# Performance work log

Hardware: AMD Instinct MI355X
Metric: run time of the kernel (lower is better)

## Reference

```python
import jax, jax.numpy as jnp
import numpy as np

N = 20000      # nodes
E = 320000     # edges (before self loops)
F_IN = 256     # num_node_features
H = 8          # heads
C = 64         # dim_h per head
B = 64         # graphs in batch
NC = 10        # num_classes
HID = H * C    # 512


def setup_inputs() -> dict:
    key = jax.random.key(0)
    ks = jax.random.split(key, 20)
    def glorot(k, shape, fan):
        return jax.random.normal(k, shape, jnp.float32) / np.sqrt(fan)
    inp = {
        'x': jax.random.normal(ks[0], (N, F_IN), jnp.float32),
        'edge_index': jax.random.randint(ks[1], (2, E), 0, N),
        'batch': jnp.sort(jax.random.randint(ks[2], (N,), 0, B)),
        # conv1: F_IN -> H*C
        'W1': glorot(ks[3], (F_IN, HID), F_IN),
        'a_src1': glorot(ks[4], (H, C), C),
        'a_dst1': glorot(ks[5], (H, C), C),
        'b1': jnp.zeros((HID,), jnp.float32),
        # conv2: HID -> H*C
        'W2': glorot(ks[6], (HID, HID), HID),
        'a_src2': glorot(ks[7], (H, C), C),
        'a_dst2': glorot(ks[8], (H, C), C),
        'b2': jnp.zeros((HID,), jnp.float32),
        # conv3: HID -> H*C
        'W3': glorot(ks[9], (HID, HID), HID),
        'a_src3': glorot(ks[10], (H, C), C),
        'a_dst3': glorot(ks[11], (H, C), C),
        'b3': jnp.zeros((HID,), jnp.float32),
        # final classifier
        'Wl': glorot(ks[12], (HID, NC), HID),
        'bl': jnp.zeros((NC,), jnp.float32),
    }
    return inp


def _gat_conv(x, src, dst, W, a_src, a_dst, b):
    """PyG GATConv (concat=True, negative_slope=0.2). src/dst include self loops."""
    xt = (x @ W).reshape(-1, H, C)                      # [N, H, C]
    al_s = jnp.einsum('nhc,hc->nh', xt, a_src)          # [N, H]
    al_d = jnp.einsum('nhc,hc->nh', xt, a_dst)
    e = jax.nn.leaky_relu(al_s[src] + al_d[dst], 0.2)   # [E', H]
    m = jax.ops.segment_max(e, dst, num_segments=N)     # segment softmax (stable)
    m = jax.lax.stop_gradient(jnp.where(jnp.isfinite(m), m, 0.0))
    p = jnp.exp(e - m[dst])
    s = jax.ops.segment_sum(p, dst, num_segments=N)
    alpha = p / (s[dst] + 1e-16)                        # [E', H]
    msg = xt[src] * alpha[..., None]                    # [E', H, C]
    out = jax.ops.segment_sum(msg, dst, num_segments=N) # [N, H, C]
    return out.reshape(-1, HID) + b


def reference(x, edge_index, batch, W1, a_src1, a_dst1, b1,
              W2, a_src2, a_dst2, b2, W3, a_src3, a_dst3, b3, Wl, bl):
    loop = jnp.arange(N, dtype=edge_index.dtype)
    src = jnp.concatenate([edge_index[0], loop])        # add_self_loops=True
    dst = jnp.concatenate([edge_index[1], loop])

    h = jax.nn.elu(_gat_conv(x, src, dst, W1, a_src1, a_dst1, b1))
    h = jax.nn.elu(_gat_conv(h, src, dst, W2, a_src2, a_dst2, b2))
    h = jax.nn.elu(_gat_conv(h, src, dst, W3, a_src3, a_dst3, b3))

    # global mean pool over graphs
    cnt = jax.ops.segment_sum(jnp.ones((N,), h.dtype), batch, num_segments=B)
    hG = jax.ops.segment_sum(h, batch, num_segments=B) / jnp.clip(cnt, 1.0)[:, None]

    # dropout p=0.5 is identity in eval mode
    logits = hG @ Wl + bl
    return hG, jax.nn.softmax(logits, axis=1)
```

## Files before the change

### kernel.cpp

```cpp
#include <hip/hip_runtime.h>
#include <hip/hip_bf16.h>
#include <math.h>

#define N_NODES  20000
#define E_EDGES  320000
#define E_TOT    (E_EDGES + N_NODES)
#define F_INF    256
#define HEADS    8
#define CDIM     64
#define HID      512
#define B_GRAPHS 64
#define NCLS     10
#define M_PAD    20096
#define NSCAN    20

typedef __attribute__((ext_vector_type(8))) short short8;
typedef __attribute__((ext_vector_type(4))) float f32x4;

__device__ inline unsigned short f2bf(float x) {
    unsigned u = __builtin_bit_cast(unsigned, x);
    u += 0x7fff + ((u >> 16) & 1);
    return (unsigned short)(u >> 16);
}
__device__ inline float bf2f(unsigned short h) {
    unsigned u = ((unsigned)h) << 16;
    return __builtin_bit_cast(float, u);
}

#define GLOAD_LDS16(g, l) __builtin_amdgcn_global_load_lds(                     \
        (const __attribute__((address_space(1))) void*)(g),                     \
        (__attribute__((address_space(3))) void*)(l), 16, 0, 0)

__global__ __launch_bounds__(256) void zero_ints(int* p, int n) {
    int i = blockIdx.x * 256 + threadIdx.x;
    if (i < n) p[i] = 0;
}

__global__ __launch_bounds__(256) void zero_pad_rows(unsigned short* hi, unsigned short* lo) {
    int i = blockIdx.x * 256 + threadIdx.x;
    const int tot = (M_PAD - N_NODES) * HID;
    if (i < tot) {
        hi[(size_t)N_NODES * HID + i] = 0;
        lo[(size_t)N_NODES * HID + i] = 0;
    }
}

__global__ __launch_bounds__(256) void split_pad(const float* __restrict__ src,
                                                 unsigned short* __restrict__ hi,
                                                 unsigned short* __restrict__ lo,
                                                 int M, int K, long total) {
    long i = ((long)blockIdx.x * 256 + threadIdx.x) * 4;
    if (i >= total) return;
    int row = (int)(i / K);
    float4 v = make_float4(0.f, 0.f, 0.f, 0.f);
    if (row < M) v = *(const float4*)(src + i);
    ushort4 h, l;
    h.x = f2bf(v.x); l.x = f2bf(v.x - bf2f(h.x));
    h.y = f2bf(v.y); l.y = f2bf(v.y - bf2f(h.y));
    h.z = f2bf(v.z); l.z = f2bf(v.z - bf2f(h.z));
    h.w = f2bf(v.w); l.w = f2bf(v.w - bf2f(h.w));
    *(ushort4*)(hi + i) = h;
    *(ushort4*)(lo + i) = l;
}

__global__ __launch_bounds__(256) void transpose_split_B(const float* __restrict__ B,
                                                         unsigned short* __restrict__ Bthi,
                                                         unsigned short* __restrict__ Btlo,
                                                         int K) {
    __shared__ float t[32][33];
    int n0 = blockIdx.x * 32, k0 = blockIdx.y * 32;
    int tx = threadIdx.x & 31, ty = threadIdx.x >> 5;
    for (int i = ty; i < 32; i += 8) t[i][tx] = B[(size_t)(k0 + i) * HID + n0 + tx];
    __syncthreads();
    for (int i = ty; i < 32; i += 8) {
        float v = t[tx][i];
        unsigned short h = f2bf(v);
        unsigned short l = f2bf(v - bf2f(h));
        Bthi[(size_t)(n0 + i) * K + k0 + tx] = h;
        Btlo[(size_t)(n0 + i) * K + k0 + tx] = l;
    }
}

__global__ __launch_bounds__(256) void gemm_mfma(const unsigned short* __restrict__ Ahi,
                                                 const unsigned short* __restrict__ Alo,
                                                 const unsigned short* __restrict__ Bhi,
                                                 const unsigned short* __restrict__ Blo,
                                                 const float* __restrict__ a_src,
                                                 const float* __restrict__ a_dst,
                                                 unsigned short* __restrict__ xtb,
                                                 float* __restrict__ al_s,
                                                 float* __restrict__ al_d,
                                                 int M, int K) {
    __shared__ short AsHi[4096], AsLo[4096], BsHi[4096], BsLo[4096];
    const int tid = threadIdx.x;
    const int w = tid >> 6, lane = tid & 63;
    const int wr = w >> 1, wc = w & 1;
    const int row0 = blockIdx.x * 128, col0 = blockIdx.y * 128;

    long offA[2], offB[2];
    int ldsU[2];
#pragma unroll
    for (int i = 0; i < 2; ++i) {
        int u = w * 128 + i * 64 + lane;
        int row = u >> 2;
        int kg = (u & 3) ^ (row & 3);
        offA[i] = ((long)(row0 + row) * K + kg * 8) * 2;
        offB[i] = ((long)(col0 + row) * K + kg * 8) * 2;
        ldsU[i] = (w * 128 + i * 64) * 8;
    }

    const int r16 = lane & 15, kg = lane >> 4;
    int aOff[4], bOff[4];
#pragma unroll
    for (int i = 0; i < 4; ++i) {
        int row = wr * 64 + i * 16 + r16;
        aOff[i] = (row * 4 + (kg ^ (row & 3))) * 16;
        int col = wc * 64 + i * 16 + r16;
        bOff[i] = (col * 4 + (kg ^ (col & 3))) * 16;
    }

    const char* pAhi = (const char*)Ahi;
    const char* pAlo = (const char*)Alo;
    const char* pBhi = (const char*)Bhi;
    const char* pBlo = (const char*)Blo;

    f32x4 acc[4][4] = {};

    for (int kk = 0; kk < K; kk += 32) {
        long kb = (long)kk * 2;
        __syncthreads();
#pragma unroll
        for (int i = 0; i < 2; ++i) {
            GLOAD_LDS16(pAhi + offA[i] + kb, AsHi + ldsU[i]);
            GLOAD_LDS16(pAlo + offA[i] + kb, AsLo + ldsU[i]);
            GLOAD_LDS16(pBhi + offB[i] + kb, BsHi + ldsU[i]);
            GLOAD_LDS16(pBlo + offB[i] + kb, BsLo + ldsU[i]);
        }
        __syncthreads();

        short8 ah[4], al[4], bh[4], bl[4];
#pragma unroll
        for (int i = 0; i < 4; ++i) {
            ah[i] = *(const short8*)((const char*)AsHi + aOff[i]);
            al[i] = *(const short8*)((const char*)AsLo + aOff[i]);
            bh[i] = *(const short8*)((const char*)BsHi + bOff[i]);
            bl[i] = *(const short8*)((const char*)BsLo + bOff[i]);
        }
#pragma unroll
        for (int i = 0; i < 4; ++i)
#pragma unroll
            for (int j = 0; j < 4; ++j) {
                acc[i][j] = __builtin_amdgcn_mfma_f32_16x16x32_bf16(ah[i], bh[j], acc[i][j], 0, 0, 0);
                acc[i][j] = __builtin_amdgcn_mfma_f32_16x16x32_bf16(ah[i], bl[j], acc[i][j], 0, 0, 0);
                acc[i][j] = __builtin_amdgcn_mfma_f32_16x16x32_bf16(al[i], bh[j], acc[i][j], 0, 0, 0);
            }
    }

    const int h = (col0 >> 6) + wc;
    float asv[4], adv[4];
#pragma unroll
    for (int j = 0; j < 4; ++j) {
        asv[j] = a_src[h * CDIM + j * 16 + r16];
        adv[j] = a_dst[h * CDIM + j * 16 + r16];
    }
#pragma unroll
    for (int i = 0; i < 4; ++i) {
        int rbase = row0 + wr * 64 + i * 16 + (lane >> 4) * 4;
#pragma unroll
        for (int r = 0; r < 4; ++r) {
            float ss = acc[i][0][r] * asv[0] + acc[i][1][r] * asv[1]
                     + acc[i][2][r] * asv[2] + acc[i][3][r] * asv[3];
            float dd = acc[i][0][r] * adv[0] + acc[i][1][r] * adv[1]
                     + acc[i][2][r] * adv[2] + acc[i][3][r] * adv[3];
#pragma unroll
            for (int off = 1; off < 16; off <<= 1) {
                ss += __shfl_xor(ss, off);
                dd += __shfl_xor(dd, off);
            }
            int row = rbase + r;
            if ((lane & 15) == 0 && row < M) {
                al_s[row * HEADS + h] = ss;
                al_d[row * HEADS + h] = dd;
            }
        }
#pragma unroll
        for (int j = 0; j < 4; ++j) {
            int col = col0 + wc * 64 + j * 16 + r16;
#pragma unroll
            for (int r = 0; r < 4; ++r)
                if (rbase + r < M) xtb[(size_t)(rbase + r) * HID + col] = f2bf(acc[i][j][r]);
        }
    }
}

__global__ __launch_bounds__(256) void count_edges(const int* __restrict__ ei,
                                                   int* __restrict__ counts) {
    int e = blockIdx.x * 256 + threadIdx.x;
    if (e < E_TOT) {
        int dst = (e < E_EDGES) ? ei[E_EDGES + e] : (e - E_EDGES);
        atomicAdd(&counts[dst], 1);
    }
}

__global__ __launch_bounds__(1024) void scan_local(const int* __restrict__ counts,
                                                   int* __restrict__ incl,
                                                   int* __restrict__ bsum) {
    __shared__ int s[1024];
    int tid = threadIdx.x;
    int i = blockIdx.x * 1024 + tid;
    int v = (i < N_NODES) ? counts[i] : 0;
    s[tid] = v;
    __syncthreads();
    for (int off = 1; off < 1024; off <<= 1) {
        int t = (tid >= off) ? s[tid - off] : 0;
        __syncthreads();
        s[tid] += t;
        __syncthreads();
    }
    if (i < N_NODES) incl[i] = s[tid];
    if (tid == 1023) bsum[blockIdx.x] = s[1023];
}

__global__ __launch_bounds__(64) void scan_bsums(const int* __restrict__ bsum,
                                                 int* __restrict__ bpre) {
    int lane = threadIdx.x;
    int v = (lane < NSCAN) ? bsum[lane] : 0;
    int incl = v;
#pragma unroll
    for (int off = 1; off < 32; off <<= 1) {
        int t = __shfl_up(incl, off);
        if (lane >= off) incl += t;
    }
    if (lane < NSCAN) bpre[lane] = incl - v;
}

__global__ __launch_bounds__(1024) void scan_finalize(const int* __restrict__ counts,
                                                      const int* __restrict__ incl,
                                                      const int* __restrict__ bpre,
                                                      int* __restrict__ offsets,
                                                      int* __restrict__ cursor) {
    int i = blockIdx.x * 1024 + threadIdx.x;
    if (i < N_NODES) {
        int inc = incl[i] + bpre[blockIdx.x];
        offsets[i + 1] = inc;
        cursor[i] = inc - counts[i];
    }
    if (i == 0) offsets[0] = 0;
}

__global__ __launch_bounds__(256) void scatter_edges(const int* __restrict__ ei,
                                                     int* __restrict__ cursor,
                                                     int* __restrict__ csr) {
    int e = blockIdx.x * 256 + threadIdx.x;
    if (e < E_TOT) {
        int dst = (e < E_EDGES) ? ei[E_EDGES + e] : (e - E_EDGES);
        int pos = atomicAdd(&cursor[dst], 1);
        csr[pos] = e;
    }
}

__global__ __launch_bounds__(256) void gat_aggregate4(const unsigned short* __restrict__ xtb,
                                                      const float* __restrict__ al_s,
                                                      const float* __restrict__ al_d,
                                                      const int* __restrict__ offsets,
                                                      const int* __restrict__ csr,
                                                      const int* __restrict__ ei,
                                                      const float* __restrict__ bias,
                                                      unsigned short* __restrict__ outHi,
                                                      unsigned short* __restrict__ outLo) {
    const int lane = threadIdx.x & 63;
    const int n = blockIdx.x * 4 + (threadIdx.x >> 6);
    const int h = lane >> 3;
    const int c0 = lane * 8;
    const int beg = offsets[n];
    const int deg = offsets[n + 1] - beg;
    const float aldv = al_d[n * HEADS + h];

    float acc[8] = {};
    float psum = 0.f;

#pragma unroll 4
    for (int i = 0; i < deg; ++i) {
        int e = csr[beg + i];
        int srcn = (e < E_EDGES) ? ei[e] : (e - E_EDGES);
        float ev = al_s[srcn * HEADS + h] + aldv;
        ev = (ev >= 0.f) ? ev : 0.2f * ev;
        float p = expf(ev);
        psum += p;
        short8 row = *(const short8*)(xtb + (size_t)srcn * HID + c0);
#pragma unroll
        for (int j = 0; j < 8; ++j)
            acc[j] = fmaf(p, bf2f((unsigned short)row[j]), acc[j]);
    }

    const float inv = 1.f / (psum + 1e-16f);
    float4 b0 = *(const float4*)(bias + c0);
    float4 b1 = *(const float4*)(bias + c0 + 4);
    float bv[8] = { b0.x, b0.y, b0.z, b0.w, b1.x, b1.y, b1.z, b1.w };
    short8 h8, l8;
#pragma unroll
    for (int j = 0; j < 8; ++j) {
        float v = acc[j] * inv + bv[j];
        v = (v > 0.f) ? v : expm1f(v);
        unsigned short hi = f2bf(v);
        h8[j] = (short)hi;
        l8[j] = (short)f2bf(v - bf2f(hi));
    }
    size_t o = (size_t)n * HID + c0;
    *(short8*)(outHi + o) = h8;
    *(short8*)(outLo + o) = l8;
}

__global__ __launch_bounds__(128) void find_bounds(const int* __restrict__ batch,
                                                   int* __restrict__ bounds) {
    int b = threadIdx.x;
    if (b <= B_GRAPHS) {
        int lo = 0, hi = N_NODES;
        while (lo < hi) {
            int mid = (lo + hi) >> 1;
            if (batch[mid] < b) lo = mid + 1; else hi = mid;
        }
        bounds[b] = lo;
    }
}

__global__ __launch_bounds__(256) void pool_partial(const unsigned short* __restrict__ hHi,
                                                    const unsigned short* __restrict__ hLo,
                                                    const int* __restrict__ bounds,
                                                    float* __restrict__ partial) {
    const int b = blockIdx.x, y = blockIdx.y, k = blockIdx.z;
    const int s = bounds[b], cnt = bounds[b + 1] - s;
    const int ns = s + (cnt * k) / 4;
    const int ne = s + (cnt * (k + 1)) / 4;
    const int t = threadIdx.x;
    const int chp = t & 31;
    const int nl = t >> 5;

    float a0 = 0.f, a1 = 0.f;
    for (int n = ns + nl; n < ne; n += 8) {
        size_t off = (size_t)n * HID + y * 64 + chp * 2;
        unsigned vh = *(const unsigned*)(hHi + off);
        unsigned vl = *(const unsigned*)(hLo + off);
        a0 += bf2f((unsigned short)(vh & 0xffff)) + bf2f((unsigned short)(vl & 0xffff));
        a1 += bf2f((unsigned short)(vh >> 16)) + bf2f((unsigned short)(vl >> 16));
    }
    __shared__ float red[4][32][2];
    a0 += __shfl_xor(a0, 32);
    a1 += __shfl_xor(a1, 32);
    if ((t & 63) < 32) { red[t >> 6][chp][0] = a0; red[t >> 6][chp][1] = a1; }
    __syncthreads();
    if (t < 64) {
        int cp = t >> 1, c = t & 1;
        float v = red[0][cp][c] + red[1][cp][c] + red[2][cp][c] + red[3][cp][c];
        partial[(((size_t)k * B_GRAPHS + b) * 8 + y) * 64 + cp * 2 + c] = v;
    }
}

__global__ __launch_bounds__(512) void pool_final(const float* __restrict__ partial,
                                                  const int* __restrict__ bounds,
                                                  float* __restrict__ hG) {
    const int b = blockIdx.x, t = threadIdx.x;
    float v = 0.f;
#pragma unroll
    for (int k = 0; k < 4; ++k)
        v += partial[((size_t)k * B_GRAPHS + b) * HID + t];
    float cnt = fmaxf((float)(bounds[b + 1] - bounds[b]), 1.0f);
    hG[b * HID + t] = v / cnt;
}

__global__ __launch_bounds__(64) void classifier_kernel(const float* __restrict__ hG,
                                                        const float* __restrict__ Wl,
                                                        const float* __restrict__ bl,
                                                        float* __restrict__ outP) {
    int b = blockIdx.x;
    int tid = threadIdx.x;
    __shared__ float row[HID];
    __shared__ float logit[NCLS];
    for (int j = tid; j < HID; j += 64) row[j] = hG[b * HID + j];
    __syncthreads();
    if (tid < NCLS) {
        float acc = bl[tid];
        for (int j = 0; j < HID; ++j) acc += row[j] * Wl[j * NCLS + tid];
        logit[tid] = acc;
    }
    __syncthreads();
    if (tid == 0) {
        float mx = logit[0];
        for (int k = 1; k < NCLS; ++k) mx = fmaxf(mx, logit[k]);
        float ssum = 0.f, ex[NCLS];
        for (int k = 0; k < NCLS; ++k) { ex[k] = expf(logit[k] - mx); ssum += ex[k]; }
        for (int k = 0; k < NCLS; ++k) outP[b * NCLS + k] = ex[k] / ssum;
    }
}

extern "C" void kernel_launch(void* const* d_in, const int* in_sizes, int n_in,
                              void* d_out, int out_size, void* d_ws, size_t ws_size,
                              hipStream_t stream) {
    const float* x     = (const float*)d_in[0];
    const int*   ei    = (const int*)d_in[1];
    const int*   batch = (const int*)d_in[2];
    const float* W[3]  = { (const float*)d_in[3], (const float*)d_in[7],  (const float*)d_in[11] };
    const float* as_[3] = { (const float*)d_in[4], (const float*)d_in[8],  (const float*)d_in[12] };
    const float* ad_[3] = { (const float*)d_in[5], (const float*)d_in[9],  (const float*)d_in[13] };
    const float* bb[3] = { (const float*)d_in[6], (const float*)d_in[10], (const float*)d_in[14] };
    const float* Wl    = (const float*)d_in[15];
    const float* bl    = (const float*)d_in[16];

    char* ws = (char*)d_ws;
    unsigned short* A1hi = (unsigned short*)ws;      ws += (size_t)M_PAD * F_INF * 2;
    unsigned short* A1lo = (unsigned short*)ws;      ws += (size_t)M_PAD * F_INF * 2;
    unsigned short* A2hi = (unsigned short*)ws;      ws += (size_t)M_PAD * HID * 2;
    unsigned short* A2lo = (unsigned short*)ws;      ws += (size_t)M_PAD * HID * 2;
    unsigned short* Bthi = (unsigned short*)ws;      ws += (size_t)HID * HID * 2;
    unsigned short* Btlo = (unsigned short*)ws;      ws += (size_t)HID * HID * 2;
    unsigned short* xtb  = (unsigned short*)ws;      ws += (size_t)N_NODES * HID * 2;
    float* als  = (float*)ws;                        ws += (size_t)N_NODES * HEADS * 4;
    float* ald  = (float*)ws;                        ws += (size_t)N_NODES * HEADS * 4;
    float* partial = (float*)ws;                     ws += (size_t)4 * B_GRAPHS * HID * 4;
    int* counts  = (int*)ws;                         ws += (size_t)N_NODES * 4;
    int* incl    = (int*)ws;                         ws += (size_t)N_NODES * 4;
    int* bsum    = (int*)ws;                         ws += 32 * 4;
    int* bpre    = (int*)ws;                         ws += 32 * 4;
    int* offsets = (int*)ws;                         ws += (size_t)(N_NODES + 1) * 4;
    int* cursor  = (int*)ws;                         ws += (size_t)N_NODES * 4;
    int* csr     = (int*)ws;                         ws += (size_t)E_TOT * 4;
    int* bounds  = (int*)ws;                         ws += (size_t)(B_GRAPHS + 1) * 4;

    float* hG = (float*)d_out;
    float* probs = (float*)d_out + (size_t)B_GRAPHS * HID;

    zero_ints<<<(N_NODES + 255) / 256, 256, 0, stream>>>(counts, N_NODES);
    count_edges<<<(E_TOT + 255) / 256, 256, 0, stream>>>(ei, counts);
    scan_local<<<NSCAN, 1024, 0, stream>>>(counts, incl, bsum);
    scan_bsums<<<1, 64, 0, stream>>>(bsum, bpre);
    scan_finalize<<<NSCAN, 1024, 0, stream>>>(counts, incl, bpre, offsets, cursor);
    scatter_edges<<<(E_TOT + 255) / 256, 256, 0, stream>>>(ei, cursor, csr);
    find_bounds<<<1, 128, 0, stream>>>(batch, bounds);
    zero_pad_rows<<<((M_PAD - N_NODES) * HID + 255) / 256, 256, 0, stream>>>(A2hi, A2lo);

    dim3 ggrid(M_PAD / 128, HID / 128);

    {
        long totA = (long)M_PAD * F_INF;
        split_pad<<<(int)(totA / 4 / 256), 256, 0, stream>>>(x, A1hi, A1lo, N_NODES, F_INF, totA);
        transpose_split_B<<<dim3(HID / 32, F_INF / 32), 256, 0, stream>>>(W[0], Bthi, Btlo, F_INF);
        gemm_mfma<<<ggrid, 256, 0, stream>>>(A1hi, A1lo, Bthi, Btlo, as_[0], ad_[0],
                                             xtb, als, ald, N_NODES, F_INF);
        gat_aggregate4<<<N_NODES / 4, 256, 0, stream>>>(xtb, als, ald, offsets, csr, ei, bb[0], A2hi, A2lo);
    }

    for (int L = 1; L < 3; ++L) {
        transpose_split_B<<<dim3(HID / 32, HID / 32), 256, 0, stream>>>(W[L], Bthi, Btlo, HID);
        gemm_mfma<<<ggrid, 256, 0, stream>>>(A2hi, A2lo, Bthi, Btlo, as_[L], ad_[L],
                                             xtb, als, ald, N_NODES, HID);
        gat_aggregate4<<<N_NODES / 4, 256, 0, stream>>>(xtb, als, ald, offsets, csr, ei, bb[L], A2hi, A2lo);
    }

    {
        dim3 pgrid(B_GRAPHS, 8, 4);
        pool_partial<<<pgrid, 256, 0, stream>>>(A2hi, A2lo, bounds, partial);
        pool_final<<<B_GRAPHS, 512, 0, stream>>>(partial, bounds, hG);
    }
    classifier_kernel<<<B_GRAPHS, 64, 0, stream>>>(hG, Wl, bl, probs);
}
```

Measured before the change: 454.9 us.

## Double-buffer GEMM LDS tiles and store source ids directly in CSR

```diff
diff --git a/kernel.cpp b/kernel.cpp
--- a/kernel.cpp
+++ b/kernel.cpp
@@ -91,7 +91,7 @@
                                                  float* __restrict__ al_s,
                                                  float* __restrict__ al_d,
                                                  int M, int K) {
-    __shared__ short AsHi[4096], AsLo[4096], BsHi[4096], BsLo[4096];
+    __shared__ short AsHi[2][4096], AsLo[2][4096], BsHi[2][4096], BsLo[2][4096];
     const int tid = threadIdx.x;
     const int w = tid >> 6, lane = tid & 63;
     const int wr = w >> 1, wc = w & 1;
@@ -126,35 +126,52 @@
 
     f32x4 acc[4][4] = {};
 
-    for (int kk = 0; kk < K; kk += 32) {
-        long kb = (long)kk * 2;
-        __syncthreads();
-#pragma unroll
-        for (int i = 0; i < 2; ++i) {
-            GLOAD_LDS16(pAhi + offA[i] + kb, AsHi + ldsU[i]);
-            GLOAD_LDS16(pAlo + offA[i] + kb, AsLo + ldsU[i]);
-            GLOAD_LDS16(pBhi + offB[i] + kb, BsHi + ldsU[i]);
-            GLOAD_LDS16(pBlo + offB[i] + kb, BsLo + ldsU[i]);
-        }
-        __syncthreads();
-
-        short8 ah[4], al[4], bh[4], bl[4];
-#pragma unroll
-        for (int i = 0; i < 4; ++i) {
-            ah[i] = *(const short8*)((const char*)AsHi + aOff[i]);
-            al[i] = *(const short8*)((const char*)AsLo + aOff[i]);
-            bh[i] = *(const short8*)((const char*)BsHi + bOff[i]);
-            bl[i] = *(const short8*)((const char*)BsLo + bOff[i]);
-        }
-#pragma unroll
-        for (int i = 0; i < 4; ++i)
-#pragma unroll
-            for (int j = 0; j < 4; ++j) {
-                acc[i][j] = __builtin_amdgcn_mfma_f32_16x16x32_bf16(ah[i], bh[j], acc[i][j], 0, 0, 0);
-                acc[i][j] = __builtin_amdgcn_mfma_f32_16x16x32_bf16(ah[i], bl[j], acc[i][j], 0, 0, 0);
-                acc[i][j] = __builtin_amdgcn_mfma_f32_16x16x32_bf16(al[i], bh[j], acc[i][j], 0, 0, 0);
-            }
-    }
+#define STAGE(buf, kk) do {                                                      \
+        long kb = (long)(kk) * 64;                                               \
+        _Pragma("unroll")                                                        \
+        for (int i_ = 0; i_ < 2; ++i_) {                                         \
+            GLOAD_LDS16(pAhi + offA[i_] + kb, &AsHi[buf][ldsU[i_]]);             \
+            GLOAD_LDS16(pAlo + offA[i_] + kb, &AsLo[buf][ldsU[i_]]);             \
+            GLOAD_LDS16(pBhi + offB[i_] + kb, &BsHi[buf][ldsU[i_]]);             \
+            GLOAD_LDS16(pBlo + offB[i_] + kb, &BsLo[buf][ldsU[i_]]);             \
+        }                                                                        \
+    } while (0)
+
+#define COMPUTE(buf) do {                                                        \
+        short8 fah[4], fal[4], fbh[4], fbl[4];                                   \
+        _Pragma("unroll")                                                        \
+        for (int i_ = 0; i_ < 4; ++i_) {                                         \
+            fah[i_] = *(const short8*)((const char*)AsHi[buf] + aOff[i_]);       \
+            fal[i_] = *(const short8*)((const char*)AsLo[buf] + aOff[i_]);       \
+            fbh[i_] = *(const short8*)((const char*)BsHi[buf] + bOff[i_]);       \
+            fbl[i_] = *(const short8*)((const char*)BsLo[buf] + bOff[i_]);       \
+        }                                                                        \
+        _Pragma("unroll")                                                        \
+        for (int i_ = 0; i_ < 4; ++i_)                                           \
+            _Pragma("unroll")                                                    \
+            for (int j_ = 0; j_ < 4; ++j_) {                                     \
+                acc[i_][j_] = __builtin_amdgcn_mfma_f32_16x16x32_bf16(fah[i_], fbh[j_], acc[i_][j_], 0, 0, 0); \
+                acc[i_][j_] = __builtin_amdgcn_mfma_f32_16x16x32_bf16(fah[i_], fbl[j_], acc[i_][j_], 0, 0, 0); \
+                acc[i_][j_] = __builtin_amdgcn_mfma_f32_16x16x32_bf16(fal[i_], fbh[j_], acc[i_][j_], 0, 0, 0); \
+            }                                                                    \
+    } while (0)
+
+    const int NS = K >> 5;
+    STAGE(0, 0);
+    asm volatile("s_waitcnt vmcnt(0)" ::: "memory");
+    __builtin_amdgcn_s_barrier();
+    int cur = 0;
+    for (int t = 0; t < NS - 1; ++t) {
+        STAGE(cur ^ 1, t + 1);
+        COMPUTE(cur);
+        asm volatile("s_waitcnt vmcnt(0)" ::: "memory");
+        __builtin_amdgcn_s_barrier();
+        cur ^= 1;
+    }
+    COMPUTE(cur);
+
+#undef STAGE
+#undef COMPUTE
 
     const int h = (col0 >> 6) + wc;
     float asv[4], adv[4];
@@ -253,9 +270,11 @@
                                                      int* __restrict__ csr) {
     int e = blockIdx.x * 256 + threadIdx.x;
     if (e < E_TOT) {
-        int dst = (e < E_EDGES) ? ei[E_EDGES + e] : (e - E_EDGES);
+        int srcn, dst;
+        if (e < E_EDGES) { srcn = ei[e]; dst = ei[E_EDGES + e]; }
+        else             { srcn = dst = e - E_EDGES; }
         int pos = atomicAdd(&cursor[dst], 1);
-        csr[pos] = e;
+        csr[pos] = srcn;
     }
 }
 
@@ -264,7 +283,6 @@
                                                       const float* __restrict__ al_d,
                                                       const int* __restrict__ offsets,
                                                       const int* __restrict__ csr,
-                                                      const int* __restrict__ ei,
                                                       const float* __restrict__ bias,
                                                       unsigned short* __restrict__ outHi,
                                                       unsigned short* __restrict__ outLo) {
@@ -281,11 +299,10 @@
 
 #pragma unroll 4
     for (int i = 0; i < deg; ++i) {
-        int e = csr[beg + i];
-        int srcn = (e < E_EDGES) ? ei[e] : (e - E_EDGES);
+        int srcn = csr[beg + i];
         float ev = al_s[srcn * HEADS + h] + aldv;
         ev = (ev >= 0.f) ? ev : 0.2f * ev;
-        float p = expf(ev);
+        float p = __expf(ev);
         psum += p;
         short8 row = *(const short8*)(xtb + (size_t)srcn * HID + c0);
 #pragma unroll
@@ -446,14 +463,14 @@
         transpose_split_B<<<dim3(HID / 32, F_INF / 32), 256, 0, stream>>>(W[0], Bthi, Btlo, F_INF);
         gemm_mfma<<<ggrid, 256, 0, stream>>>(A1hi, A1lo, Bthi, Btlo, as_[0], ad_[0],
                                              xtb, als, ald, N_NODES, F_INF);
-        gat_aggregate4<<<N_NODES / 4, 256, 0, stream>>>(xtb, als, ald, offsets, csr, ei, bb[0], A2hi, A2lo);
+        gat_aggregate4<<<N_NODES / 4, 256, 0, stream>>>(xtb, als, ald, offsets, csr, bb[0], A2hi, A2lo);
     }
 
     for (int L = 1; L < 3; ++L) {
         transpose_split_B<<<dim3(HID / 32, HID / 32), 256, 0, stream>>>(W[L], Bthi, Btlo, HID);
         gemm_mfma<<<ggrid, 256, 0, stream>>>(A2hi, A2lo, Bthi, Btlo, as_[L], ad_[L],
                                              xtb, als, ald, N_NODES, HID);
-        gat_aggregate4<<<N_NODES / 4, 256, 0, stream>>>(xtb, als, ald, offsets, csr, ei, bb[L], A2hi, A2lo);
+        gat_aggregate4<<<N_NODES / 4, 256, 0, stream>>>(xtb, als, ald, offsets, csr, bb[L], A2hi, A2lo);
     }
 
     {
```

Result: faster. 436.0 us (-4.2%).

## Store source ids in CSR, remap GEMM tiles per XCD, tweak LDS swizzle

Applied to the files above, without the earlier changes.

```diff
diff --git a/kernel.cpp b/kernel.cpp
--- a/kernel.cpp
+++ b/kernel.cpp
@@ -13,6 +13,7 @@
 #define NCLS     10
 #define M_PAD    20096
 #define NSCAN    20
+#define NWG_GEMM 628
 
 typedef __attribute__((ext_vector_type(8))) short short8;
 typedef __attribute__((ext_vector_type(4))) float f32x4;
@@ -95,7 +96,11 @@
     const int tid = threadIdx.x;
     const int w = tid >> 6, lane = tid & 63;
     const int wr = w >> 1, wc = w & 1;
-    const int row0 = blockIdx.x * 128, col0 = blockIdx.y * 128;
+
+    const int xcd = blockIdx.x & 7, idx = blockIdx.x >> 3;
+    const int q = NWG_GEMM >> 3, r = NWG_GEMM & 7;
+    const int wg = (xcd < r) ? (xcd * (q + 1) + idx) : (r * (q + 1) + (xcd - r) * q + idx);
+    const int row0 = (wg >> 2) * 128, col0 = (wg & 3) * 128;
 
     long offA[2], offB[2];
     int ldsU[2];
@@ -103,7 +108,7 @@
     for (int i = 0; i < 2; ++i) {
         int u = w * 128 + i * 64 + lane;
         int row = u >> 2;
-        int kg = (u & 3) ^ (row & 3);
+        int kg = (u & 3) ^ ((row >> 1) & 3);
         offA[i] = ((long)(row0 + row) * K + kg * 8) * 2;
         offB[i] = ((long)(col0 + row) * K + kg * 8) * 2;
         ldsU[i] = (w * 128 + i * 64) * 8;
@@ -114,9 +119,9 @@
 #pragma unroll
     for (int i = 0; i < 4; ++i) {
         int row = wr * 64 + i * 16 + r16;
-        aOff[i] = (row * 4 + (kg ^ (row & 3))) * 16;
+        aOff[i] = (row * 4 + (kg ^ ((row >> 1) & 3))) * 16;
         int col = wc * 64 + i * 16 + r16;
-        bOff[i] = (col * 4 + (kg ^ (col & 3))) * 16;
+        bOff[i] = (col * 4 + (kg ^ ((col >> 1) & 3))) * 16;
     }
 
     const char* pAhi = (const char*)Ahi;
@@ -138,21 +143,21 @@
         }
         __syncthreads();
 
-        short8 ah[4], al[4], bh[4], bl[4];
+        short8 fah[4], fal[4], fbh[4], fbl[4];
 #pragma unroll
         for (int i = 0; i < 4; ++i) {
-            ah[i] = *(const short8*)((const char*)AsHi + aOff[i]);
-            al[i] = *(const short8*)((const char*)AsLo + aOff[i]);
-            bh[i] = *(const short8*)((const char*)BsHi + bOff[i]);
-            bl[i] = *(const short8*)((const char*)BsLo + bOff[i]);
+            fah[i] = *(const short8*)((const char*)AsHi + aOff[i]);
+            fal[i] = *(const short8*)((const char*)AsLo + aOff[i]);
+            fbh[i] = *(const short8*)((const char*)BsHi + bOff[i]);
+            fbl[i] = *(const short8*)((const char*)BsLo + bOff[i]);
         }
 #pragma unroll
         for (int i = 0; i < 4; ++i)
 #pragma unroll
             for (int j = 0; j < 4; ++j) {
-                acc[i][j] = __builtin_amdgcn_mfma_f32_16x16x32_bf16(ah[i], bh[j], acc[i][j], 0, 0, 0);
-                acc[i][j] = __builtin_amdgcn_mfma_f32_16x16x32_bf16(ah[i], bl[j], acc[i][j], 0, 0, 0);
-                acc[i][j] = __builtin_amdgcn_mfma_f32_16x16x32_bf16(al[i], bh[j], acc[i][j], 0, 0, 0);
+                acc[i][j] = __builtin_amdgcn_mfma_f32_16x16x32_bf16(fah[i], fbh[j], acc[i][j], 0, 0, 0);
+                acc[i][j] = __builtin_amdgcn_mfma_f32_16x16x32_bf16(fah[i], fbl[j], acc[i][j], 0, 0, 0);
+                acc[i][j] = __builtin_amdgcn_mfma_f32_16x16x32_bf16(fal[i], fbh[j], acc[i][j], 0, 0, 0);
             }
     }
 
@@ -167,17 +172,17 @@
     for (int i = 0; i < 4; ++i) {
         int rbase = row0 + wr * 64 + i * 16 + (lane >> 4) * 4;
 #pragma unroll
-        for (int r = 0; r < 4; ++r) {
-            float ss = acc[i][0][r] * asv[0] + acc[i][1][r] * asv[1]
-                     + acc[i][2][r] * asv[2] + acc[i][3][r] * asv[3];
-            float dd = acc[i][0][r] * adv[0] + acc[i][1][r] * adv[1]
-                     + acc[i][2][r] * adv[2] + acc[i][3][r] * adv[3];
+        for (int rr = 0; rr < 4; ++rr) {
+            float ss = acc[i][0][rr] * asv[0] + acc[i][1][rr] * asv[1]
+                     + acc[i][2][rr] * asv[2] + acc[i][3][rr] * asv[3];
+            float dd = acc[i][0][rr] * adv[0] + acc[i][1][rr] * adv[1]
+                     + acc[i][2][rr] * adv[2] + acc[i][3][rr] * adv[3];
 #pragma unroll
             for (int off = 1; off < 16; off <<= 1) {
                 ss += __shfl_xor(ss, off);
                 dd += __shfl_xor(dd, off);
             }
-            int row = rbase + r;
+            int row = rbase + rr;
             if ((lane & 15) == 0 && row < M) {
                 al_s[row * HEADS + h] = ss;
                 al_d[row * HEADS + h] = dd;
@@ -187,8 +192,8 @@
         for (int j = 0; j < 4; ++j) {
             int col = col0 + wc * 64 + j * 16 + r16;
 #pragma unroll
-            for (int r = 0; r < 4; ++r)
-                if (rbase + r < M) xtb[(size_t)(rbase + r) * HID + col] = f2bf(acc[i][j][r]);
+            for (int rr = 0; rr < 4; ++rr)
+                if (rbase + rr < M) xtb[(size_t)(rbase + rr) * HID + col] = f2bf(acc[i][j][rr]);
         }
     }
 }
@@ -253,9 +258,11 @@
                                                      int* __restrict__ csr) {
     int e = blockIdx.x * 256 + threadIdx.x;
     if (e < E_TOT) {
-        int dst = (e < E_EDGES) ? ei[E_EDGES + e] : (e - E_EDGES);
+        int srcn, dst;
+        if (e < E_EDGES) { srcn = ei[e]; dst = ei[E_EDGES + e]; }
+        else             { srcn = dst = e - E_EDGES; }
         int pos = atomicAdd(&cursor[dst], 1);
-        csr[pos] = e;
+        csr[pos] = srcn;
     }
 }
 
@@ -264,7 +271,6 @@
                                                       const float* __restrict__ al_d,
                                                       const int* __restrict__ offsets,
                                                       const int* __restrict__ csr,
-                                                      const int* __restrict__ ei,
                                                       const float* __restrict__ bias,
                                                       unsigned short* __restrict__ outHi,
                                                       unsigned short* __restrict__ outLo) {
@@ -281,11 +287,10 @@
 
 #pragma unroll 4
     for (int i = 0; i < deg; ++i) {
-        int e = csr[beg + i];
-        int srcn = (e < E_EDGES) ? ei[e] : (e - E_EDGES);
+        int srcn = csr[beg + i];
         float ev = al_s[srcn * HEADS + h] + aldv;
         ev = (ev >= 0.f) ? ev : 0.2f * ev;
-        float p = expf(ev);
+        float p = __expf(ev);
         psum += p;
         short8 row = *(const short8*)(xtb + (size_t)srcn * HID + c0);
 #pragma unroll
@@ -438,22 +443,20 @@
     find_bounds<<<1, 128, 0, stream>>>(batch, bounds);
     zero_pad_rows<<<((M_PAD - N_NODES) * HID + 255) / 256, 256, 0, stream>>>(A2hi, A2lo);
 
-    dim3 ggrid(M_PAD / 128, HID / 128);
-
     {
         long totA = (long)M_PAD * F_INF;
         split_pad<<<(int)(totA / 4 / 256), 256, 0, stream>>>(x, A1hi, A1lo, N_NODES, F_INF, totA);
         transpose_split_B<<<dim3(HID / 32, F_INF / 32), 256, 0, stream>>>(W[0], Bthi, Btlo, F_INF);
-        gemm_mfma<<<ggrid, 256, 0, stream>>>(A1hi, A1lo, Bthi, Btlo, as_[0], ad_[0],
-                                             xtb, als, ald, N_NODES, F_INF);
-        gat_aggregate4<<<N_NODES / 4, 256, 0, stream>>>(xtb, als, ald, offsets, csr, ei, bb[0], A2hi, A2lo);
+        gemm_mfma<<<NWG_GEMM, 256, 0, stream>>>(A1hi, A1lo, Bthi, Btlo, as_[0], ad_[0],
+                                                xtb, als, ald, N_NODES, F_INF);
+        gat_aggregate4<<<N_NODES / 4, 256, 0, stream>>>(xtb, als, ald, offsets, csr, bb[0], A2hi, A2lo);
     }
 
     for (int L = 1; L < 3; ++L) {
         transpose_split_B<<<dim3(HID / 32, HID / 32), 256, 0, stream>>>(W[L], Bthi, Btlo, HID);
-        gemm_mfma<<<ggrid, 256, 0, stream>>>(A2hi, A2lo, Bthi, Btlo, as_[L], ad_[L],
-                                             xtb, als, ald, N_NODES, HID);
-        gat_aggregate4<<<N_NODES / 4, 256, 0, stream>>>(xtb, als, ald, offsets, csr, ei, bb[L], A2hi, A2lo);
+        gemm_mfma<<<NWG_GEMM, 256, 0, stream>>>(A2hi, A2lo, Bthi, Btlo, as_[L], ad_[L],
+                                                xtb, als, ald, N_NODES, HID);
+        gat_aggregate4<<<N_NODES / 4, 256, 0, stream>>>(xtb, als, ald, offsets, csr, bb[L], A2hi, A2lo);
     }
 
     {
```

New measurement: 405.3 us. 1.12x faster.
